# Kernel optimization log

Hardware: AMD Instinct MI355X
Metric: run time of the kernel (lower is better)

## Reference

```python
import jax, jax.numpy as jnp
import numpy as np

DIM = 1024
N_HEADS = 16
HEAD_DIM = DIM // N_HEADS
B, S = 2, 2048
NEG = -1e9  # additive causal mask value (finite, safe in low precision)


def setup_inputs() -> dict:
    key = jax.random.key(0)
    k_x, k_q, k_k, k_v, k_o = jax.random.split(key, 5)
    x = jax.random.normal(k_x, (B, S, DIM), dtype=jnp.float32)
    # causal additive mask, broadcastable to [B, H, S, S]
    causal = jnp.triu(jnp.ones((S, S), dtype=bool), k=1)
    mask = jnp.where(causal, NEG, 0.0).astype(jnp.float32)[None, None]
    scale = 1.0 / np.sqrt(DIM)
    wq = jax.random.normal(k_q, (DIM, DIM), dtype=jnp.float32) * scale
    wk = jax.random.normal(k_k, (DIM, DIM), dtype=jnp.float32) * scale
    wv = jax.random.normal(k_v, (DIM, DIM), dtype=jnp.float32) * scale
    wo = jax.random.normal(k_o, (DIM, DIM), dtype=jnp.float32) * scale
    return {"x": x, "mask": mask, "wq": wq, "wk": wk, "wv": wv, "wo": wo}


def reference(x, mask, wq, wk, wv, wo):
    bs, seqlen, _ = x.shape
    # nn.Linear(y) = y @ W^T ; weights stored as (out, in)
    q = (x @ wq.T).reshape(bs, seqlen, N_HEADS, HEAD_DIM)
    k = (x @ wk.T).reshape(bs, seqlen, N_HEADS, HEAD_DIM)
    v = (x @ wv.T).reshape(bs, seqlen, N_HEADS, HEAD_DIM)
    # scores: [B, H, S, S] — intentionally materialized, as in the original
    attn = jnp.einsum('bqhd,bkhd->bhqk', q, k) / np.sqrt(HEAD_DIM)
    attn = attn + mask
    attn = jax.nn.softmax(attn, axis=-1)
    out = jnp.einsum('bhqk,bkhd->bqhd', attn, v).reshape(bs, seqlen, DIM)
    return out @ wo.T
```

## Files before the change

### kernel.cpp

```cpp
#include <hip/hip_runtime.h>

typedef __attribute__((ext_vector_type(8))) short bf16x8;
typedef __attribute__((ext_vector_type(4))) float f32x4;
typedef __attribute__((ext_vector_type(16))) float f32x16;
typedef __attribute__((ext_vector_type(4))) unsigned short u16x4;
typedef __attribute__((ext_vector_type(8))) unsigned short u16x8;

#define DIM 1024
#define SEQ 2048
#define NHEAD 16
#define HDIM 64
#define C2 0.18033688011112042f

__device__ __forceinline__ unsigned short f2bf(float f) {
  union { float f; unsigned u; } v; v.f = f;
  unsigned r = v.u + 0x7fffu + ((v.u >> 16) & 1u);
  return (unsigned short)(r >> 16);
}

__device__ __forceinline__ float bf2f(unsigned short s) {
  union { unsigned u; float f; } v; v.u = ((unsigned)s) << 16;
  return v.f;
}

__device__ __forceinline__ void gload_lds16(const void* g, void* l) {
  __builtin_amdgcn_global_load_lds(
      (const __attribute__((address_space(1))) void*)g,
      (__attribute__((address_space(3))) void*)l, 16, 0, 0);
}

__device__ __forceinline__ f32x16 mfma32(bf16x8 a, bf16x8 b, f32x16 c) {
  return __builtin_amdgcn_mfma_f32_32x32x16_bf16(a, b, c, 0, 0, 0);
}

__device__ __forceinline__ unsigned cvtpk(float lo, float hi) {
  unsigned r;
  asm("v_cvt_pk_bf16_f32 %0, %1, %2" : "=v"(r) : "v"(lo), "v"(hi));
  return r;
}

__global__ void f2bf_all(const float* __restrict__ x, const float* __restrict__ wq,
                         const float* __restrict__ wk, const float* __restrict__ wv,
                         const float* __restrict__ wo, unsigned short* __restrict__ xb,
                         unsigned short* __restrict__ wb) {
  int blk = blockIdx.x;
  const float* src;
  unsigned short* dst;
  int rb;
  if (blk < 4096) { src = x; dst = xb; rb = blk; }
  else {
    int w = (blk - 4096) >> 10;
    src = w == 0 ? wq : w == 1 ? wk : w == 2 ? wv : wo;
    dst = wb + (size_t)w * 1048576;
    rb = (blk - 4096) & 1023;
  }
  int i = rb * 256 + threadIdx.x;
  float4 v = ((const float4*)src)[i];
  u16x4 o;
  o[0] = f2bf(v.x); o[1] = f2bf(v.y); o[2] = f2bf(v.z); o[3] = f2bf(v.w);
  ((u16x4*)dst)[i] = o;
}

__global__ __launch_bounds__(256) void gemm3(
    const unsigned short* __restrict__ xb,
    const unsigned short* __restrict__ wb,
    unsigned short* __restrict__ qkv) {
  __shared__ unsigned short As[2][4096];
  __shared__ unsigned short Bs[2][4096];
  const int bz = blockIdx.x;
  const unsigned short *A, *B;
  unsigned short* C;
  int m0, n0, ldc;
  float cscale = 1.0f;
  if (bz < 512) {
    int xcd = bz & 7, inner = bz >> 3;
    int mm = inner & 3, n = (inner >> 2) & 7, w = inner >> 5;
    m0 = (xcd * 4 + mm) * 128; n0 = n * 128;
    A = xb; B = wb + w * 1048576; C = qkv + w * 4194304; ldc = 1024;
    if (w == 0) cscale = C2;
  } else {
    int idx = bz - 512;
    int xcd = idx & 7, inner = idx >> 3;
    int tt = inner & 3, mv = inner >> 2;
    m0 = mv * 128; n0 = (xcd * 4 + tt) * 128;
    A = wb + 2 * 1048576; B = xb; C = qkv + 2 * 4194304; ldc = 4096;
  }
  const int tid = threadIdx.x;
  const int wv = tid >> 6, lane = tid & 63;
  const int g = lane >> 4, l16 = lane & 15;
  const int wm = (wv >> 1) * 64, wn = (wv & 1) * 64;
  const int sro = lane >> 2, sc4 = lane & 3;
  f32x4 acc[4][4] = {};

#define GSTAGE(IT, BUF)                                                        \
  {                                                                            \
    const int kt = (IT) * 32;                                                  \
    _Pragma("unroll")                                                          \
    for (int s = 0; s < 2; ++s) {                                              \
      int r = wv * 32 + s * 16 + sro;                                          \
      int cd = sc4 ^ ((r >> 1) & 3);                                           \
      gload_lds16(A + (long long)(m0 + r) * 1024 + kt + cd * 8,                \
                  &As[BUF][wv * 1024 + s * 512]);                              \
      gload_lds16(B + (long long)(n0 + r) * 1024 + kt + cd * 8,                \
                  &Bs[BUF][wv * 1024 + s * 512]);                              \
    }                                                                          \
  }

  GSTAGE(0, 0);
  __syncthreads();

  for (int it = 0; it < 32; ++it) {
    const int buf = it & 1;
    if (it + 1 < 32) GSTAGE(it + 1, buf ^ 1);
    bf16x8 af[4], bfr[4];
#pragma unroll
    for (int mf = 0; mf < 4; ++mf) {
      int row = wm + mf * 16 + l16;
      af[mf] = *(const bf16x8*)((const char*)&As[buf][0] + row * 64 +
                                ((g ^ ((row >> 1) & 3)) << 4));
    }
#pragma unroll
    for (int nf = 0; nf < 4; ++nf) {
      int row = wn + nf * 16 + l16;
      bfr[nf] = *(const bf16x8*)((const char*)&Bs[buf][0] + row * 64 +
                                 ((g ^ ((row >> 1) & 3)) << 4));
    }
#pragma unroll
    for (int mf = 0; mf < 4; ++mf)
#pragma unroll
      for (int nf = 0; nf < 4; ++nf)
        acc[mf][nf] = __builtin_amdgcn_mfma_f32_16x16x32_bf16(
            af[mf], bfr[nf], acc[mf][nf], 0, 0, 0);
    __syncthreads();
  }

#pragma unroll
  for (int mf = 0; mf < 4; ++mf)
#pragma unroll
    for (int nf = 0; nf < 4; ++nf)
#pragma unroll
      for (int r = 0; r < 4; ++r) {
        long long m = m0 + wm + mf * 16 + g * 4 + r;
        long long n = n0 + wn + nf * 16 + l16;
        C[m * ldc + n] = f2bf(acc[mf][nf][r] * cscale);
      }
}

__global__ __launch_bounds__(256) void gemm_out(
    const unsigned short* __restrict__ A,
    const unsigned short* __restrict__ B,
    float* __restrict__ C) {
  __shared__ unsigned short As[2][4096];
  __shared__ unsigned short Bs[2][4096];
  const int tid = threadIdx.x;
  const int wv = tid >> 6, lane = tid & 63;
  const int g = lane >> 4, l16 = lane & 15;
  const int m0 = blockIdx.y * 128, n0 = blockIdx.x * 128;
  const int wm = (wv >> 1) * 64, wn = (wv & 1) * 64;
  const int sro = lane >> 2, sc4 = lane & 3;
  f32x4 acc[4][4] = {};

#define OSTAGE(IT, BUF)                                                        \
  {                                                                            \
    const int kt = (IT) * 32;                                                  \
    _Pragma("unroll")                                                          \
    for (int s = 0; s < 2; ++s) {                                              \
      int r = wv * 32 + s * 16 + sro;                                          \
      int cd = sc4 ^ ((r >> 1) & 3);                                           \
      gload_lds16(A + (long long)(m0 + r) * 1024 + kt + cd * 8,                \
                  &As[BUF][wv * 1024 + s * 512]);                              \
      gload_lds16(B + (long long)(n0 + r) * 1024 + kt + cd * 8,                \
                  &Bs[BUF][wv * 1024 + s * 512]);                              \
    }                                                                          \
  }

  OSTAGE(0, 0);
  __syncthreads();

  for (int it = 0; it < 32; ++it) {
    const int buf = it & 1;
    if (it + 1 < 32) OSTAGE(it + 1, buf ^ 1);
    bf16x8 af[4], bfr[4];
#pragma unroll
    for (int mf = 0; mf < 4; ++mf) {
      int row = wm + mf * 16 + l16;
      af[mf] = *(const bf16x8*)((const char*)&As[buf][0] + row * 64 +
                                ((g ^ ((row >> 1) & 3)) << 4));
    }
#pragma unroll
    for (int nf = 0; nf < 4; ++nf) {
      int row = wn + nf * 16 + l16;
      bfr[nf] = *(const bf16x8*)((const char*)&Bs[buf][0] + row * 64 +
                                 ((g ^ ((row >> 1) & 3)) << 4));
    }
#pragma unroll
    for (int mf = 0; mf < 4; ++mf)
#pragma unroll
      for (int nf = 0; nf < 4; ++nf)
        acc[mf][nf] = __builtin_amdgcn_mfma_f32_16x16x32_bf16(
            af[mf], bfr[nf], acc[mf][nf], 0, 0, 0);
    __syncthreads();
  }

#pragma unroll
  for (int mf = 0; mf < 4; ++mf)
#pragma unroll
    for (int nf = 0; nf < 4; ++nf)
#pragma unroll
      for (int r = 0; r < 4; ++r) {
        long long m = m0 + wm + mf * 16 + g * 4 + r;
        long long n = n0 + wn + nf * 16 + l16;
        C[m * 1024 + n] = acc[mf][nf][r];
      }
}

__global__ __launch_bounds__(256, 4) void attn_kernel(
    const unsigned short* __restrict__ Qg,
    const unsigned short* __restrict__ Kg,
    const unsigned short* __restrict__ VTg,
    unsigned short* __restrict__ Og,
    unsigned short* __restrict__ pacc,
    float* __restrict__ pml) {
  __shared__ unsigned short Kls[2][4096];
  __shared__ unsigned short Vls[2][4096];

  const int tid = threadIdx.x;
  const int wv = tid >> 6, lane = tid & 63;
  const int l32 = lane & 31, hi = lane >> 5;
  const int h = blockIdx.y, b = blockIdx.z;

  const int i = blockIdx.x;
  int qt, c, cn;
  if (i < 16)      { qt = 15 - (i >> 2); c = i & 3; cn = 4; }
  else if (i < 28) { int j = i - 16; qt = 11 - j / 3; c = j % 3; cn = 3; }
  else if (i < 36) { int j = i - 28; qt = 7 - ((j >> 1)); c = j & 1; cn = 2; }
  else             { qt = 39 - i; c = 0; cn = 1; }

  const int nt = 2 * qt + 2;
  const int t0 = c * 8;
  const int tb = min(t0 + 8, nt);
  const int umax = 4 * qt + wv;

  const int q = qt * 128 + wv * 32 + l32;
  const long long bh = (long long)b * SEQ * DIM + h * HDIM;
  const long long vbase = (long long)h * HDIM * 4096 + b * SEQ;

  const unsigned short* Qrow = Qg + (long long)(b * SEQ + q) * DIM + h * HDIM;
  bf16x8 qf[4];
#pragma unroll
  for (int ds = 0; ds < 4; ++ds)
    qf[ds] = *(const bf16x8*)(Qrow + ds * 16 + hi * 8);

  bf16x8 ones;
#pragma unroll
  for (int j = 0; j < 8; ++j) ones[j] = (short)0x3F80;

  f32x16 acc0 = {}, acc1 = {}, lacc = {};

  const int sr = lane >> 3, sc = lane & 7;
#define STAGE(T, BUF)                                                          \
  {                                                                            \
    const int kv0s = (T) * 64;                                                 \
    _Pragma("unroll")                                                          \
    for (int s = 0; s < 2; ++s) {                                              \
      int jj = wv * 2 + s;                                                     \
      int r = jj * 8 + sr;                                                     \
      int cs = (sc ^ (r & 7)) * 8;                                             \
      gload_lds16(Kg + bh + (long long)(kv0s + r) * DIM + cs,                  \
                  &Kls[BUF][jj * 512]);                                        \
      gload_lds16(VTg + vbase + (long long)r * 4096 + kv0s + cs,               \
                  &Vls[BUF][jj * 512]);                                        \
    }                                                                          \
  }

  STAGE(t0, 0);
  __syncthreads();

  for (int t = t0; t < tb; ++t) {
    const int buf = (t - t0) & 1;
    if (t + 1 < tb) STAGE(t + 1, buf ^ 1);

#pragma unroll
    for (int s = 0; s < 2; ++s) {
      const int u = 2 * t + s;
      if (u <= umax) {
        f32x16 sv = {};
        __builtin_amdgcn_s_setprio(1);
#pragma unroll
        for (int ds = 0; ds < 4; ++ds) {
          const int cbk = (((ds << 1) | hi) ^ (l32 & 7)) * 16;
          bf16x8 kf = *(const bf16x8*)((const char*)&Kls[buf][0] +
                                       (s * 32 + l32) * 128 + cbk);
          sv = mfma32(kf, qf[ds], sv);
        }
        __builtin_amdgcn_s_setprio(0);

        if (u == umax) {
#pragma unroll
          for (int r = 0; r < 16; ++r) {
            int kw = (r & 3) + 8 * (r >> 2) + 4 * hi;
            if (kw > l32) sv[r] = -1e30f;
          }
        }

#pragma unroll
        for (int r = 0; r < 16; ++r) sv[r] = exp2f(sv[r]);

        __builtin_amdgcn_s_setprio(1);
#pragma unroll
        for (int kk = 0; kk < 2; ++kk) {
          const int base = kk * 8;
          unsigned a0 = cvtpk(sv[base + 0], sv[base + 1]);
          unsigned a1 = cvtpk(sv[base + 2], sv[base + 3]);
          unsigned a2 = cvtpk(sv[base + 4], sv[base + 5]);
          unsigned a3 = cvtpk(sv[base + 6], sv[base + 7]);
          asm("v_permlane32_swap_b32 %0, %1" : "+v"(a0), "+v"(a2));
          asm("v_permlane32_swap_b32 %0, %1" : "+v"(a1), "+v"(a3));
          union { unsigned u4[4]; bf16x8 v; } pf;
          pf.u4[0] = a0; pf.u4[1] = a1; pf.u4[2] = a2; pf.u4[3] = a3;
          const int slice = 2 * s + kk;
          const int cbv = (((slice << 1) | hi) ^ (l32 & 7)) * 16;
          bf16x8 v0 = *(const bf16x8*)((const char*)&Vls[buf][0] + l32 * 128 + cbv);
          bf16x8 v1 = *(const bf16x8*)((const char*)&Vls[buf][0] + (32 + l32) * 128 + cbv);
          acc0 = mfma32(v0, pf.v, acc0);
          acc1 = mfma32(v1, pf.v, acc1);
          lacc = mfma32(ones, pf.v, lacc);
        }
        __builtin_amdgcn_s_setprio(0);
      }
    }
    __syncthreads();
  }

  const float l_run = lacc[0];

  if (cn == 1) {
    const float inv_l = 1.0f / l_run;
    unsigned short* Orow = Og + (long long)(b * SEQ + q) * DIM + h * HDIM;
#pragma unroll
    for (int dblk = 0; dblk < 2; ++dblk) {
#pragma unroll
      for (int g4 = 0; g4 < 4; ++g4) {
        u16x4 o;
#pragma unroll
        for (int jv = 0; jv < 4; ++jv) {
          float v = (dblk ? acc1[g4 * 4 + jv] : acc0[g4 * 4 + jv]) * inv_l;
          o[jv] = f2bf(v);
        }
        *(u16x4*)(Orow + dblk * 32 + 8 * g4 + 4 * hi) = o;
      }
    }
  } else {
    const int sbase = qt < 8 ? 2 * (qt - 4) : qt < 12 ? 8 + 3 * (qt - 8) : 20 + 4 * (qt - 12);
    const int slot = (b * NHEAD + h) * 36 + sbase + c;
    unsigned short* pbase = pacc + (size_t)slot * 8192 + (wv * 32 + l32) * 64;
#pragma unroll
    for (int dblk = 0; dblk < 2; ++dblk) {
#pragma unroll
      for (int g4 = 0; g4 < 4; ++g4) {
        u16x4 o;
#pragma unroll
        for (int jv = 0; jv < 4; ++jv)
          o[jv] = f2bf(dblk ? acc1[g4 * 4 + jv] : acc0[g4 * 4 + jv]);
        *(u16x4*)(pbase + dblk * 32 + 8 * g4 + 4 * hi) = o;
      }
    }
    if (hi == 0) pml[slot * 128 + wv * 32 + l32] = l_run;
  }
}

__global__ __launch_bounds__(256) void attn_merge(
    const unsigned short* __restrict__ pacc,
    const float* __restrict__ pml,
    unsigned short* __restrict__ Og) {
  const int qt = 4 + blockIdx.x;
  const int h = blockIdx.y, b = blockIdx.z;
  const int cn = (qt >> 2) + 1;
  const int sbase = qt < 8 ? 2 * (qt - 4) : qt < 12 ? 8 + 3 * (qt - 8) : 20 + 4 * (qt - 12);
  const int base_slot = (b * NHEAD + h) * 36 + sbase;
  const int t = threadIdx.x;
  const int ql = t >> 1, d0 = (t & 1) * 32;

  float L = 0.f;
#pragma unroll
  for (int cc = 0; cc < 4; ++cc)
    if (cc < cn) L += pml[(base_slot + cc) * 128 + ql];
  const float invL = 1.0f / L;

  float o[32] = {};
#pragma unroll
  for (int cc = 0; cc < 4; ++cc)
    if (cc < cn) {
      const unsigned short* p = pacc + (size_t)(base_slot + cc) * 8192 + ql * 64 + d0;
#pragma unroll
      for (int k = 0; k < 32; k += 8) {
        u16x8 v = *(const u16x8*)(p + k);
#pragma unroll
        for (int jv = 0; jv < 8; ++jv) o[k + jv] += bf2f(v[jv]);
      }
    }

  const int q = qt * 128 + ql;
  unsigned short* orow = Og + (size_t)(b * SEQ + q) * DIM + h * HDIM + d0;
#pragma unroll
  for (int k = 0; k < 32; k += 8) {
    u16x8 ov;
#pragma unroll
    for (int jv = 0; jv < 8; ++jv) ov[jv] = f2bf(o[k + jv] * invL);
    *(u16x8*)(orow + k) = ov;
  }
}

extern "C" void kernel_launch(void* const* d_in, const int* in_sizes, int n_in,
                              void* d_out, int out_size, void* d_ws, size_t ws_size,
                              hipStream_t stream) {
  const float* x   = (const float*)d_in[0];
  const float* wq  = (const float*)d_in[2];
  const float* wk  = (const float*)d_in[3];
  const float* wv_ = (const float*)d_in[4];
  const float* wo  = (const float*)d_in[5];

  unsigned short* xb  = (unsigned short*)d_ws;
  unsigned short* wb  = xb + (size_t)4096 * 1024;
  unsigned short* qkv = wb + (size_t)4 * 1024 * 1024;
  unsigned short* ao  = qkv + (size_t)3 * 4096 * 1024;
  unsigned short* pacc = ao + (size_t)4096 * 1024;
  float* pml = (float*)(pacc + (size_t)1152 * 8192);

  f2bf_all<<<8192, 256, 0, stream>>>(x, wq, wk, wv_, wo, xb, wb);

  gemm3<<<768, 256, 0, stream>>>(xb, wb, qkv);

  attn_kernel<<<dim3(40, 16, 2), 256, 0, stream>>>(
      qkv, qkv + 4194304, qkv + 2 * 4194304, ao, pacc, pml);

  attn_merge<<<dim3(12, 16, 2), 256, 0, stream>>>(pacc, pml, ao);

  gemm_out<<<dim3(8, 32, 1), 256, 0, stream>>>(ao, wb + 3145728, (float*)d_out);
}
```

Baseline: 127.4 us.

## Prefetch two stages ahead with explicit vmcnt waits in GEMM and attention loops

Restructures the double-buffered load pipeline in the QKV GEMM, output GEMM and attention kernels. Two stages are issued up front, and each iteration waits only with a partial s_waitcnt vmcnt(4) plus a raw barrier instead of __syncthreads, which drains all outstanding loads. The next-next stage is issued after compute, and sched_barrier fences stop the compiler from moving loads across the phases. This keeps one stage of global-to-LDS loads in flight during compute. The cost is a redundant reload of the last tile at the tail, and correctness now depends on the hand-counted vmcnt value matching the number of loads per stage.

```diff
diff --git a/kernel.cpp b/kernel.cpp
--- a/kernel.cpp
+++ b/kernel.cpp
@@ -11,6 +11,11 @@
 #define NHEAD 16
 #define HDIM 64
 #define C2 0.18033688011112042f
+
+#define WAIT_VM4() asm volatile("s_waitcnt vmcnt(4)" ::: "memory")
+#define WAIT_VM0() asm volatile("s_waitcnt vmcnt(0)" ::: "memory")
+#define BAR() __builtin_amdgcn_s_barrier()
+#define SCHEDB() __builtin_amdgcn_sched_barrier(0)
 
 __device__ __forceinline__ unsigned short f2bf(float f) {
   union { float f; unsigned u; } v; v.f = f;
@@ -107,11 +112,13 @@
   }
 
   GSTAGE(0, 0);
-  __syncthreads();
+  GSTAGE(1, 1);
 
   for (int it = 0; it < 32; ++it) {
     const int buf = it & 1;
-    if (it + 1 < 32) GSTAGE(it + 1, buf ^ 1);
+    WAIT_VM4();
+    BAR();
+    SCHEDB();
     bf16x8 af[4], bfr[4];
 #pragma unroll
     for (int mf = 0; mf < 4; ++mf) {
@@ -131,7 +138,12 @@
       for (int nf = 0; nf < 4; ++nf)
         acc[mf][nf] = __builtin_amdgcn_mfma_f32_16x16x32_bf16(
             af[mf], bfr[nf], acc[mf][nf], 0, 0, 0);
-    __syncthreads();
+    SCHEDB();
+    BAR();
+    if (it + 1 < 32) {
+      int nx = (it + 2 < 32) ? it + 2 : 31;
+      GSTAGE(nx, buf);
+    }
   }
 
 #pragma unroll
@@ -175,11 +187,13 @@
   }
 
   OSTAGE(0, 0);
-  __syncthreads();
+  OSTAGE(1, 1);
 
   for (int it = 0; it < 32; ++it) {
     const int buf = it & 1;
-    if (it + 1 < 32) OSTAGE(it + 1, buf ^ 1);
+    WAIT_VM4();
+    BAR();
+    SCHEDB();
     bf16x8 af[4], bfr[4];
 #pragma unroll
     for (int mf = 0; mf < 4; ++mf) {
@@ -199,7 +213,12 @@
       for (int nf = 0; nf < 4; ++nf)
         acc[mf][nf] = __builtin_amdgcn_mfma_f32_16x16x32_bf16(
             af[mf], bfr[nf], acc[mf][nf], 0, 0, 0);
-    __syncthreads();
+    SCHEDB();
+    BAR();
+    if (it + 1 < 32) {
+      int nx = (it + 2 < 32) ? it + 2 : 31;
+      OSTAGE(nx, buf);
+    }
   }
 
 #pragma unroll
@@ -250,6 +269,7 @@
 #pragma unroll
   for (int ds = 0; ds < 4; ++ds)
     qf[ds] = *(const bf16x8*)(Qrow + ds * 16 + hi * 8);
+  WAIT_VM0();
 
   bf16x8 ones;
 #pragma unroll
@@ -274,11 +294,13 @@
   }
 
   STAGE(t0, 0);
-  __syncthreads();
+  { int nx = (t0 + 1 < tb) ? t0 + 1 : tb - 1; STAGE(nx, 1); }
 
   for (int t = t0; t < tb; ++t) {
     const int buf = (t - t0) & 1;
-    if (t + 1 < tb) STAGE(t + 1, buf ^ 1);
+    WAIT_VM4();
+    BAR();
+    SCHEDB();
 
 #pragma unroll
     for (int s = 0; s < 2; ++s) {
@@ -329,7 +351,12 @@
         __builtin_amdgcn_s_setprio(0);
       }
     }
-    __syncthreads();
+    SCHEDB();
+    BAR();
+    if (t + 1 < tb) {
+      int nx = (t + 2 < tb) ? t + 2 : tb - 1;
+      STAGE(nx, buf);
+    }
   }
 
   const float l_run = lacc[0];
```

After: 117.5 us. 1.08x faster.
